# Performance work log

Measured on AMD Instinct MI355X. Metric: run time of the kernel, lower is better.

Reference implementation:

```python
import jax, jax.numpy as jnp
import numpy as np

B, S, C = 4, 4096, 128
C4 = C // 4  # q/k channels
OUT = 128    # == in_features, required by value @ weight


def setup_inputs() -> dict:
    key = jax.random.key(0)
    ks = jax.random.split(key, 9)
    stdv = 1.0 / np.sqrt(OUT)
    u = lambda k, shape, s: jax.random.uniform(k, shape, jnp.float32, -s, s)
    kaiming = lambda k, shape: u(k, shape, float(1.0 / np.sqrt(shape[1])))
    return {
        "x": jax.random.normal(ks[0], (B, S, C), jnp.float32),
        "weight": u(ks[1], (C, OUT), stdv),      # GCN weight [in, out]
        "bias": u(ks[2], (OUT,), stdv),
        "wq": kaiming(ks[3], (C4, C)),           # conv1d k=1 == linear [out_ch, in_ch]
        "bq": u(ks[4], (C4,), float(1.0 / np.sqrt(C))),
        "wk": kaiming(ks[5], (C4, C)),
        "bk": u(ks[6], (C4,), float(1.0 / np.sqrt(C))),
        "wv": kaiming(ks[7], (OUT, C)),
        "bv": u(ks[8], (OUT,), float(1.0 / np.sqrt(C))),
    }


def reference(x, weight, bias, wq, bq, wk, bk, wv, bv):
    # conv1d with kernel_size=1 == per-position linear projection
    q = jnp.einsum("bsc,qc->bsq", x, wq) + bq        # [B,S,C4] (query, pre-permute it is [B,C4,S])
    k = jnp.einsum("bsc,qc->bsq", x, wk) + bk        # [B,S,C4]
    # scores[i,j] = key_i . query_j  (unscaled), softmax over j
    scores = jnp.einsum("bic,bjc->bij", k, q)        # [B,S,S]
    adj = jax.nn.softmax(scores, axis=-1)
    v = jnp.einsum("bsc,oc->bso", x, wv) + bv        # [B,S,OUT]
    support = jnp.einsum("bso,ou->bsu", v, weight)   # [B,S,OUT]
    out = jnp.einsum("bij,bju->biu", adj, support)   # [B,S,OUT]
    return out + bias
```

## Files before the change

kernel.cpp:

```cpp
#include <hip/hip_runtime.h>

#define NB   4
#define SEQ  4096
#define CIN  128
#define C4D  32
#define OUTC 128
#define LOG2E 1.44269504f

typedef __attribute__((ext_vector_type(8))) short bf16x8;
typedef __attribute__((ext_vector_type(4))) float f32x4;

__device__ __forceinline__ short f2bf(float f) {
  union { float f; unsigned u; } v; v.f = f;
  unsigned r = v.u + 0x7FFFu + ((v.u >> 16) & 1u);
  return (short)(r >> 16);
}

__device__ __forceinline__ unsigned cvt_pk_bf16(float lo, float hi) {
  unsigned r;
  asm("v_cvt_pk_bf16_f32 %0, %1, %2" : "=v"(r) : "v"(lo), "v"(hi));
  return r;
}

__device__ __forceinline__ float fast_exp2(float x) {
  float r;
  asm("v_exp_f32 %0, %1" : "=v"(r) : "v"(x));
  return r;
}

__device__ __forceinline__ f32x4 mfma16(bf16x8 a, bf16x8 b, f32x4 c) {
  return __builtin_amdgcn_mfma_f32_16x16x32_bf16(a, b, c, 0, 0, 0);
}

__device__ __forceinline__ void gload_lds16(const short* g, short* l) {
  __builtin_amdgcn_global_load_lds(
      (const __attribute__((address_space(1))) void*)(g),
      (__attribute__((address_space(3))) void*)(l), 16, 0, 0);
}

__global__ void k_fuse(const float* __restrict__ wq, const float* __restrict__ wk,
                       const float* __restrict__ wv, const float* __restrict__ weight,
                       const float* __restrict__ bv,
                       short* __restrict__ wqb, short* __restrict__ wkb,
                       short* __restrict__ wfT, float* __restrict__ bfu) {
  int u = blockIdx.x, c = threadIdx.x;
  float a0 = 0.f, a1 = 0.f, a2 = 0.f, a3 = 0.f;
  for (int o = 0; o < OUTC; o += 4) {
    a0 += wv[(o + 0) * CIN + c] * weight[(o + 0) * OUTC + u];
    a1 += wv[(o + 1) * CIN + c] * weight[(o + 1) * OUTC + u];
    a2 += wv[(o + 2) * CIN + c] * weight[(o + 2) * OUTC + u];
    a3 += wv[(o + 3) * CIN + c] * weight[(o + 3) * OUTC + u];
  }
  wfT[u * CIN + c] = f2bf((a0 + a1) + (a2 + a3));
  if (u < C4D) {
    wqb[u * CIN + c] = f2bf(wq[u * CIN + c]);
    wkb[u * CIN + c] = f2bf(wk[u * CIN + c]);
  }
  if (c == 0) {
    float b0 = 0.f, b1 = 0.f;
    for (int o = 0; o < OUTC; o += 2) {
      b0 += bv[o] * weight[o * OUTC + u];
      b1 += bv[o + 1] * weight[(o + 1) * OUTC + u];
    }
    bfu[u] = b0 + b1;
  }
}

__device__ __forceinline__ int wswz(int byte) {
  return byte ^ (((byte >> 8) & 7) << 4);
}

__global__ __launch_bounds__(256) void k_proj(
    const float* __restrict__ x, const float* __restrict__ bq, const float* __restrict__ bk,
    const short* __restrict__ wall, const float* __restrict__ bfu,
    short* __restrict__ ql, short* __restrict__ kb, short* __restrict__ vfb) {
  const int tid = threadIdx.x;
  const int wid = tid >> 6, lane = tid & 63;
  const int lo = lane & 15, g = lane >> 4;
  const int p0 = blockIdx.x * 64 + wid * 16;

  __shared__ __align__(16) short WL[24576];
#pragma unroll
  for (int i = 0; i < 12; ++i) {
    bf16x8 v = *(const bf16x8*)(wall + i * 2048 + tid * 8);
    *(bf16x8*)((char*)WL + wswz((i * 2048 + tid * 8) * 2)) = v;
  }
  __syncthreads();

  auto wfrag = [&](int idx) -> bf16x8 {
    return *(const bf16x8*)((char*)WL + wswz(idx * 2));
  };

  f32x4 aq[2] = {}, ak[2] = {}, as_[8] = {};

#pragma unroll
  for (int kk = 0; kk < 4; ++kk) {
    const float* xp = x + (size_t)(p0 + lo) * CIN + kk * 32 + g * 8;
    float4 xa = *(const float4*)xp;
    float4 xb = *(const float4*)(xp + 4);
    bf16x8 af;
    af[0] = f2bf(xa.x); af[1] = f2bf(xa.y); af[2] = f2bf(xa.z); af[3] = f2bf(xa.w);
    af[4] = f2bf(xb.x); af[5] = f2bf(xb.y); af[6] = f2bf(xb.z); af[7] = f2bf(xb.w);
#pragma unroll
    for (int n = 0; n < 2; ++n) {
      bf16x8 bq_ = wfrag((n * 16 + lo) * CIN + kk * 32 + g * 8);
      aq[n] = mfma16(af, bq_, aq[n]);
      bf16x8 bk_ = wfrag(4096 + (n * 16 + lo) * CIN + kk * 32 + g * 8);
      ak[n] = mfma16(af, bk_, ak[n]);
    }
#pragma unroll
    for (int n = 0; n < 8; ++n) {
      bf16x8 bs = wfrag(8192 + (n * 16 + lo) * CIN + kk * 32 + g * 8);
      as_[n] = mfma16(af, bs, as_[n]);
    }
  }

#pragma unroll
  for (int n = 0; n < 2; ++n) {
    float bqv = bq[n * 16 + lo], bkv = bk[n * 16 + lo];
    int u = n * 16 + lo;
#pragma unroll
    for (int r = 0; r < 4; ++r) {
      int p = p0 + 4 * g + r;
      int bb = p >> 12, s = p & (SEQ - 1);
      ql[(size_t)bb * (SEQ * 32) + (size_t)(s >> 5) * 1024 + ((s >> 4) & 1) * 512 +
         (u >> 3) * 128 + (s & 15) * 8 + (u & 7)] = f2bf(aq[n][r] + bqv);
      kb[(size_t)p * C4D + u] = f2bf((ak[n][r] + bkv) * LOG2E);
    }
  }
  {
    const int p = p0 + 4 * g;
    const int bb = p >> 12, s = p & (SEQ - 1);
#pragma unroll
    for (int n = 0; n < 8; ++n) {
      int u = n * 16 + lo;
      float bvv = bfu[u];
      uint2 w;
      w.x = cvt_pk_bf16(as_[n][0] + bvv, as_[n][1] + bvv);
      w.y = cvt_pk_bf16(as_[n][2] + bvv, as_[n][3] + bvv);
      *(uint2*)&vfb[(size_t)bb * (SEQ * 128) + (size_t)(s >> 5) * 4096 + (u >> 4) * 512 +
                    ((s >> 2) & 3) * 128 + (u & 15) * 8 + ((s >> 4) & 1) * 4] = w;
    }
  }
}

__global__ __launch_bounds__(512, 2) void k_attn(
    const short* __restrict__ ql, const short* __restrict__ kb,
    const short* __restrict__ vfb, const float* __restrict__ bias,
    float* __restrict__ out) {
  const int tid = threadIdx.x;
  const int wid = tid >> 6, lane = tid & 63;
  const int lo = lane & 15, g = lane >> 4;
  const int bid = blockIdx.x;
  const int xb = ((bid & 7) << 5) | (bid >> 3);
  const int b = xb >> 6;
  const int iw = (xb & 63) * 64;

  __shared__ __align__(16) char smem[133120];
  short* Vs = (short*)smem;
  float* LDSF = (float*)smem;

  const short* qB = ql + (size_t)b * (SEQ * 32) + (size_t)wid * 16384;
  const short* vB = vfb + (size_t)b * (SEQ * 128) + (size_t)wid * 65536;
  short* Vw = Vs + wid * 8192;

  bf16x8 kf[4];
#pragma unroll
  for (int c = 0; c < 4; ++c)
    kf[c] = *(const bf16x8*)(kb + (size_t)(b * SEQ + iw + 16 * c + lo) * C4D + g * 8);

  f32x4 o[4][8];
#pragma unroll
  for (int c = 0; c < 4; ++c)
#pragma unroll
    for (int n = 0; n < 8; ++n) o[c][n] = (f32x4){0.f, 0.f, 0.f, 0.f};

  float ma[4] = {-3e38f, -3e38f, -3e38f, -3e38f};
  float la[4] = {0.f, 0.f, 0.f, 0.f};
  const f32x4 zf = {0.f, 0.f, 0.f, 0.f};

  bf16x8 pf[4];

  bf16x8 qf0 = *(const bf16x8*)(qB + lane * 8);
  bf16x8 qf1 = *(const bf16x8*)(qB + 512 + lane * 8);
#pragma unroll
  for (int n = 0; n < 8; ++n)
    gload_lds16(vB + n * 512 + lane * 8, Vw + n * 512);

#pragma unroll 2
  for (int t = 0; t < 16; ++t) {
    const int cur = t & 1, nxt = cur ^ 1;

    f32x4 s0[4], s1[4];
    float tm[4];
    __builtin_amdgcn_s_setprio(1);
#pragma unroll
    for (int c = 0; c < 4; ++c) {
      s0[c] = mfma16(qf0, kf[c], zf);
      s1[c] = mfma16(qf1, kf[c], zf);
    }
    __builtin_amdgcn_s_setprio(0);
#pragma unroll
    for (int c = 0; c < 4; ++c) {
      tm[c] = fmaxf(fmaxf(fmaxf(s0[c][0], s0[c][1]), fmaxf(s0[c][2], s0[c][3])),
                    fmaxf(fmaxf(s1[c][0], s1[c][1]), fmaxf(s1[c][2], s1[c][3])));
    }

    if (t + 1 < 16) {
      const short* qt = qB + (size_t)(t + 1) * 1024;
      qf0 = *(const bf16x8*)(qt + lane * 8);
      qf1 = *(const bf16x8*)(qt + 512 + lane * 8);
      const short* vn = vB + (size_t)(t + 1) * 4096;
      short* vd = Vw + nxt * 4096;
#pragma unroll
      for (int n = 0; n < 8; ++n)
        gload_lds16(vn + n * 512 + lane * 8, vd + n * 512);
    }

    bool need = (tm[0] > ma[0] + 11.5f) | (tm[1] > ma[1] + 11.5f) |
                (tm[2] > ma[2] + 11.5f) | (tm[3] > ma[3] + 11.5f);
    if (__any(need)) {
#pragma unroll
      for (int c = 0; c < 4; ++c) {
        float rowm = fmaxf(tm[c], __shfl_xor(tm[c], 16, 64));
        rowm = fmaxf(rowm, __shfl_xor(rowm, 32, 64));
        float mnew = fmaxf(ma[c], rowm);
        float scale = fast_exp2(ma[c] - mnew);
        la[c] *= scale;
        float sc[4];
#pragma unroll
        for (int r = 0; r < 4; ++r) sc[r] = __shfl(scale, 4 * g + r, 64);
#pragma unroll
        for (int n = 0; n < 8; ++n)
#pragma unroll
          for (int r = 0; r < 4; ++r) o[c][n][r] *= sc[r];
        ma[c] = mnew;
      }
    }

#pragma unroll
    for (int c = 0; c < 4; ++c) {
      float p[8];
#pragma unroll
      for (int r = 0; r < 4; ++r) {
        p[r]     = fast_exp2(s0[c][r] - ma[c]);
        p[4 + r] = fast_exp2(s1[c][r] - ma[c]);
      }
      la[c] += (p[0] + p[1]) + (p[2] + p[3]) + ((p[4] + p[5]) + (p[6] + p[7]));
      union { bf16x8 v8; unsigned u[4]; } pk;
      pk.u[0] = cvt_pk_bf16(p[0], p[1]);
      pk.u[1] = cvt_pk_bf16(p[2], p[3]);
      pk.u[2] = cvt_pk_bf16(p[4], p[5]);
      pk.u[3] = cvt_pk_bf16(p[6], p[7]);
      pf[c] = pk.v8;
    }

    asm volatile("s_waitcnt vmcnt(10)" ::: "memory");

    const short* vt = Vw + cur * 4096;
    __builtin_amdgcn_s_setprio(1);
#pragma unroll
    for (int n = 0; n < 8; ++n) {
      bf16x8 vfr = *(const bf16x8*)(vt + n * 512 + lane * 8);
      o[0][n] = mfma16(pf[0], vfr, o[0][n]);
      o[1][n] = mfma16(pf[1], vfr, o[1][n]);
      o[2][n] = mfma16(pf[2], vfr, o[2][n]);
      o[3][n] = mfma16(pf[3], vfr, o[3][n]);
    }
    __builtin_amdgcn_s_setprio(0);
  }

#pragma unroll
  for (int c = 0; c < 4; ++c) {
    la[c] += __shfl_xor(la[c], 16, 64);
    la[c] += __shfl_xor(la[c], 32, 64);
  }

  __syncthreads();

  auto write_slot = [&](int s) {
    float* OSs = LDSF + s * 8192;
#pragma unroll
    for (int c = 0; c < 4; ++c)
#pragma unroll
      for (int n = 0; n < 8; ++n)
        *(f32x4*)&OSs[(c * 8 + n) * 256 + lane * 4] = o[c][n];
    if (lane < 16) {
#pragma unroll
      for (int c = 0; c < 4; ++c) {
        LDSF[32768 + s * 64 + c * 16 + lo] = ma[c];
        LDSF[33024 + s * 64 + c * 16 + lo] = la[c];
      }
    }
  };
  auto merge_slot = [&](int s) {
    float* OSs = LDSF + s * 8192;
#pragma unroll
    for (int c = 0; c < 4; ++c) {
      float ms = LDSF[32768 + s * 64 + c * 16 + lo];
      float ls = LDSF[33024 + s * 64 + c * 16 + lo];
      float M = fmaxf(ma[c], ms);
      float eo = fast_exp2(ma[c] - M), es = fast_exp2(ms - M);
      la[c] = eo * la[c] + es * ls;
      ma[c] = M;
      float eor[4], esr[4];
#pragma unroll
      for (int r = 0; r < 4; ++r) {
        eor[r] = __shfl(eo, 4 * g + r, 64);
        esr[r] = __shfl(es, 4 * g + r, 64);
      }
#pragma unroll
      for (int n = 0; n < 8; ++n) {
        f32x4 v = *(f32x4*)&OSs[(c * 8 + n) * 256 + lane * 4];
#pragma unroll
        for (int r = 0; r < 4; ++r)
          o[c][n][r] = eor[r] * o[c][n][r] + esr[r] * v[r];
      }
    }
  };

  if (wid >= 4) write_slot(wid - 4);
  __syncthreads();
  if (wid < 4) merge_slot(wid);
  __syncthreads();
  if (wid == 1) write_slot(0);
  if (wid == 3) write_slot(1);
  __syncthreads();
  if (wid == 0) merge_slot(0);
  if (wid == 2) merge_slot(1);
  __syncthreads();
  if (wid == 2) write_slot(0);
  __syncthreads();
  if (wid == 0) {
    merge_slot(0);
    float* outp = out + (size_t)(b * SEQ + iw) * OUTC;
#pragma unroll
    for (int c = 0; c < 4; ++c) {
      float ia = 1.f / la[c];
      float lir[4];
#pragma unroll
      for (int r = 0; r < 4; ++r) lir[r] = __shfl(ia, 4 * g + r, 64);
#pragma unroll
      for (int n = 0; n < 8; ++n) {
        float bu = bias[n * 16 + lo];
#pragma unroll
        for (int r = 0; r < 4; ++r)
          outp[(size_t)(c * 16 + 4 * g + r) * OUTC + n * 16 + lo] =
              o[c][n][r] * lir[r] + bu;
      }
    }
  }
}

extern "C" void kernel_launch(void* const* d_in, const int* in_sizes, int n_in,
                              void* d_out, int out_size, void* d_ws, size_t ws_size,
                              hipStream_t stream) {
  (void)in_sizes; (void)n_in; (void)out_size; (void)ws_size;
  const float* x      = (const float*)d_in[0];
  const float* weight = (const float*)d_in[1];
  const float* bias   = (const float*)d_in[2];
  const float* wq     = (const float*)d_in[3];
  const float* bq     = (const float*)d_in[4];
  const float* wk     = (const float*)d_in[5];
  const float* bk     = (const float*)d_in[6];
  const float* wv     = (const float*)d_in[7];
  const float* bv     = (const float*)d_in[8];
  float* out = (float*)d_out;

  char* ws = (char*)d_ws;
  short* kbuf = (short*)(ws);
  short* vfb  = (short*)(ws + ((size_t)1 << 20));
  short* qlb  = (short*)(ws + ((size_t)5 << 20));
  short* wqb  = (short*)(ws + ((size_t)6 << 20));
  short* wkb  = (short*)(ws + ((size_t)6 << 20) + 8192);
  short* wfT  = (short*)(ws + ((size_t)6 << 20) + 16384);
  float* bfu  = (float*)(ws + ((size_t)6 << 20) + 49152);

  hipLaunchKernelGGL(k_fuse, dim3(OUTC), dim3(CIN), 0, stream,
                     wq, wk, wv, weight, bv, wqb, wkb, wfT, bfu);
  hipLaunchKernelGGL(k_proj, dim3(NB * SEQ / 64), dim3(256), 0, stream,
                     x, bq, bk, wqb , bfu, qlb, kbuf, vfb);
  hipLaunchKernelGGL(k_attn, dim3(NB * SEQ / 64), dim3(512), 0, stream,
                     qlb, kbuf, vfb, bias, out);
}
```

Baseline: 53.06 us.

## Shrink attention tiles to 32 rows, 4 waves, load V directly to registers

The attention kernel now processes 32 query rows per block with 4 waves instead of 64 rows with 8 waves, doubling the grid. Each wave handles 1024 keys over 32 iterations. V fragments are read straight from global memory into registers instead of being staged through LDS with async global-to-LDS loads. This aims to raise occupancy and cut LDS use, but each V tile is now reused by only 2 row blocks per wave rather than 4, which roughly doubles global and L2 traffic for V and removes the explicit prefetch overlap.

```diff
diff --git a/kernel.cpp b/kernel.cpp
--- a/kernel.cpp
+++ b/kernel.cpp
@@ -30,12 +30,6 @@
 
 __device__ __forceinline__ f32x4 mfma16(bf16x8 a, bf16x8 b, f32x4 c) {
   return __builtin_amdgcn_mfma_f32_16x16x32_bf16(a, b, c, 0, 0, 0);
-}
-
-__device__ __forceinline__ void gload_lds16(const short* g, short* l) {
-  __builtin_amdgcn_global_load_lds(
-      (const __attribute__((address_space(1))) void*)(g),
-      (__attribute__((address_space(3))) void*)(l), 16, 0, 0);
 }
 
 __global__ void k_fuse(const float* __restrict__ wq, const float* __restrict__ wk,
@@ -144,7 +138,7 @@
   }
 }
 
-__global__ __launch_bounds__(512, 2) void k_attn(
+__global__ __launch_bounds__(256, 3) void k_attn(
     const short* __restrict__ ql, const short* __restrict__ kb,
     const short* __restrict__ vfb, const float* __restrict__ bias,
     float* __restrict__ out) {
@@ -152,76 +146,68 @@
   const int wid = tid >> 6, lane = tid & 63;
   const int lo = lane & 15, g = lane >> 4;
   const int bid = blockIdx.x;
-  const int xb = ((bid & 7) << 5) | (bid >> 3);
-  const int b = xb >> 6;
-  const int iw = (xb & 63) * 64;
-
-  __shared__ __align__(16) char smem[133120];
-  short* Vs = (short*)smem;
-  float* LDSF = (float*)smem;
-
-  const short* qB = ql + (size_t)b * (SEQ * 32) + (size_t)wid * 16384;
-  const short* vB = vfb + (size_t)b * (SEQ * 128) + (size_t)wid * 65536;
-  short* Vw = Vs + wid * 8192;
-
-  bf16x8 kf[4];
-#pragma unroll
-  for (int c = 0; c < 4; ++c)
+  const int xb = ((bid & 7) << 6) | (bid >> 3);
+  const int b = xb >> 7;
+  const int iw = (xb & 127) * 32;
+
+  __shared__ float OS[2][4096];
+  __shared__ float MS[2][32], LS[2][32];
+
+  const short* qB = ql + (size_t)b * (SEQ * 32) + (size_t)wid * 32768;
+  const short* vB = vfb + (size_t)b * (SEQ * 128) + (size_t)wid * 131072;
+
+  bf16x8 kf[2];
+#pragma unroll
+  for (int c = 0; c < 2; ++c)
     kf[c] = *(const bf16x8*)(kb + (size_t)(b * SEQ + iw + 16 * c + lo) * C4D + g * 8);
 
-  f32x4 o[4][8];
-#pragma unroll
-  for (int c = 0; c < 4; ++c)
+  f32x4 o[2][8];
+#pragma unroll
+  for (int c = 0; c < 2; ++c)
 #pragma unroll
     for (int n = 0; n < 8; ++n) o[c][n] = (f32x4){0.f, 0.f, 0.f, 0.f};
 
-  float ma[4] = {-3e38f, -3e38f, -3e38f, -3e38f};
-  float la[4] = {0.f, 0.f, 0.f, 0.f};
+  float ma[2] = {-3e38f, -3e38f};
+  float la[2] = {0.f, 0.f};
   const f32x4 zf = {0.f, 0.f, 0.f, 0.f};
 
-  bf16x8 pf[4];
+  bf16x8 pf[2];
 
   bf16x8 qf0 = *(const bf16x8*)(qB + lane * 8);
   bf16x8 qf1 = *(const bf16x8*)(qB + 512 + lane * 8);
-#pragma unroll
-  for (int n = 0; n < 8; ++n)
-    gload_lds16(vB + n * 512 + lane * 8, Vw + n * 512);
-
-#pragma unroll 2
-  for (int t = 0; t < 16; ++t) {
-    const int cur = t & 1, nxt = cur ^ 1;
-
-    f32x4 s0[4], s1[4];
-    float tm[4];
+
+  for (int t = 0; t < 32; ++t) {
+    bf16x8 vfr[8];
+    const short* vt = vB + (size_t)t * 4096;
+#pragma unroll
+    for (int n = 0; n < 8; ++n)
+      vfr[n] = *(const bf16x8*)(vt + n * 512 + lane * 8);
+
+    f32x4 s0[2], s1[2];
+    float tm[2];
     __builtin_amdgcn_s_setprio(1);
 #pragma unroll
-    for (int c = 0; c < 4; ++c) {
+    for (int c = 0; c < 2; ++c) {
       s0[c] = mfma16(qf0, kf[c], zf);
       s1[c] = mfma16(qf1, kf[c], zf);
     }
     __builtin_amdgcn_s_setprio(0);
 #pragma unroll
-    for (int c = 0; c < 4; ++c) {
+    for (int c = 0; c < 2; ++c) {
       tm[c] = fmaxf(fmaxf(fmaxf(s0[c][0], s0[c][1]), fmaxf(s0[c][2], s0[c][3])),
                     fmaxf(fmaxf(s1[c][0], s1[c][1]), fmaxf(s1[c][2], s1[c][3])));
     }
 
-    if (t + 1 < 16) {
+    if (t + 1 < 32) {
       const short* qt = qB + (size_t)(t + 1) * 1024;
       qf0 = *(const bf16x8*)(qt + lane * 8);
       qf1 = *(const bf16x8*)(qt + 512 + lane * 8);
-      const short* vn = vB + (size_t)(t + 1) * 4096;
-      short* vd = Vw + nxt * 4096;
-#pragma unroll
-      for (int n = 0; n < 8; ++n)
-        gload_lds16(vn + n * 512 + lane * 8, vd + n * 512);
-    }
-
-    bool need = (tm[0] > ma[0] + 11.5f) | (tm[1] > ma[1] + 11.5f) |
-                (tm[2] > ma[2] + 11.5f) | (tm[3] > ma[3] + 11.5f);
+    }
+
+    bool need = (tm[0] > ma[0] + 11.5f) | (tm[1] > ma[1] + 11.5f);
     if (__any(need)) {
 #pragma unroll
-      for (int c = 0; c < 4; ++c) {
+      for (int c = 0; c < 2; ++c) {
         float rowm = fmaxf(tm[c], __shfl_xor(tm[c], 16, 64));
         rowm = fmaxf(rowm, __shfl_xor(rowm, 32, 64));
         float mnew = fmaxf(ma[c], rowm);
@@ -239,7 +225,7 @@
     }
 
 #pragma unroll
-    for (int c = 0; c < 4; ++c) {
+    for (int c = 0; c < 2; ++c) {
       float p[8];
 #pragma unroll
       for (int r = 0; r < 4; ++r) {
@@ -255,50 +241,40 @@
       pf[c] = pk.v8;
     }
 
-    asm volatile("s_waitcnt vmcnt(10)" ::: "memory");
-
-    const short* vt = Vw + cur * 4096;
     __builtin_amdgcn_s_setprio(1);
 #pragma unroll
     for (int n = 0; n < 8; ++n) {
-      bf16x8 vfr = *(const bf16x8*)(vt + n * 512 + lane * 8);
-      o[0][n] = mfma16(pf[0], vfr, o[0][n]);
-      o[1][n] = mfma16(pf[1], vfr, o[1][n]);
-      o[2][n] = mfma16(pf[2], vfr, o[2][n]);
-      o[3][n] = mfma16(pf[3], vfr, o[3][n]);
+      o[0][n] = mfma16(pf[0], vfr[n], o[0][n]);
+      o[1][n] = mfma16(pf[1], vfr[n], o[1][n]);
     }
     __builtin_amdgcn_s_setprio(0);
   }
 
 #pragma unroll
-  for (int c = 0; c < 4; ++c) {
+  for (int c = 0; c < 2; ++c) {
     la[c] += __shfl_xor(la[c], 16, 64);
     la[c] += __shfl_xor(la[c], 32, 64);
   }
 
-  __syncthreads();
-
   auto write_slot = [&](int s) {
-    float* OSs = LDSF + s * 8192;
-#pragma unroll
-    for (int c = 0; c < 4; ++c)
+#pragma unroll
+    for (int c = 0; c < 2; ++c)
 #pragma unroll
       for (int n = 0; n < 8; ++n)
-        *(f32x4*)&OSs[(c * 8 + n) * 256 + lane * 4] = o[c][n];
+        *(f32x4*)&OS[s][(c * 8 + n) * 256 + lane * 4] = o[c][n];
     if (lane < 16) {
 #pragma unroll
-      for (int c = 0; c < 4; ++c) {
-        LDSF[32768 + s * 64 + c * 16 + lo] = ma[c];
-        LDSF[33024 + s * 64 + c * 16 + lo] = la[c];
+      for (int c = 0; c < 2; ++c) {
+        MS[s][c * 16 + lo] = ma[c];
+        LS[s][c * 16 + lo] = la[c];
       }
     }
   };
   auto merge_slot = [&](int s) {
-    float* OSs = LDSF + s * 8192;
-#pragma unroll
-    for (int c = 0; c < 4; ++c) {
-      float ms = LDSF[32768 + s * 64 + c * 16 + lo];
-      float ls = LDSF[33024 + s * 64 + c * 16 + lo];
+#pragma unroll
+    for (int c = 0; c < 2; ++c) {
+      float ms = MS[s][c * 16 + lo];
+      float ls = LS[s][c * 16 + lo];
       float M = fmaxf(ma[c], ms);
       float eo = fast_exp2(ma[c] - M), es = fast_exp2(ms - M);
       la[c] = eo * la[c] + es * ls;
@@ -311,7 +287,7 @@
       }
 #pragma unroll
       for (int n = 0; n < 8; ++n) {
-        f32x4 v = *(f32x4*)&OSs[(c * 8 + n) * 256 + lane * 4];
+        f32x4 v = *(f32x4*)&OS[s][(c * 8 + n) * 256 + lane * 4];
 #pragma unroll
         for (int r = 0; r < 4; ++r)
           o[c][n][r] = eor[r] * o[c][n][r] + esr[r] * v[r];
@@ -319,10 +295,6 @@
     }
   };
 
-  if (wid >= 4) write_slot(wid - 4);
-  __syncthreads();
-  if (wid < 4) merge_slot(wid);
-  __syncthreads();
   if (wid == 1) write_slot(0);
   if (wid == 3) write_slot(1);
   __syncthreads();
@@ -335,7 +307,7 @@
     merge_slot(0);
     float* outp = out + (size_t)(b * SEQ + iw) * OUTC;
 #pragma unroll
-    for (int c = 0; c < 4; ++c) {
+    for (int c = 0; c < 2; ++c) {
       float ia = 1.f / la[c];
       float lir[4];
 #pragma unroll
@@ -380,6 +352,6 @@
                      wq, wk, wv, weight, bv, wqb, wkb, wfT, bfu);
   hipLaunchKernelGGL(k_proj, dim3(NB * SEQ / 64), dim3(256), 0, stream,
                      x, bq, bk, wqb , bfu, qlb, kbuf, vfb);
-  hipLaunchKernelGGL(k_attn, dim3(NB * SEQ / 64), dim3(512), 0, stream,
+  hipLaunchKernelGGL(k_attn, dim3(NB * SEQ / 32), dim3(256), 0, stream,
                      qlb, kbuf, vfb, bias, out);
 }
```

Result: faster. 50.30 us (-5.2%).
